# Kernel optimization log

Measured on AMD Instinct MI355X. Metric: run time of the kernel, lower is better.

Reference implementation:

```python
import jax, jax.numpy as jnp
import numpy as np

N = 50000      # nodes
E = 400000     # edges
NODE_IN = 16
EDGE_IN = 8
H = 4          # heads (layer 1)
C = 64         # hidden_dim
HC = H * C     # 256


def setup_inputs() -> dict:
    key = jax.random.key(0)
    ks = iter(jax.random.split(key, 48))
    def rn(shape, s=0.05):
        return jax.random.normal(next(ks), shape, jnp.float32) * s
    x = jax.random.normal(next(ks), (N, NODE_IN), jnp.float32)
    edge_index = jax.random.randint(next(ks), (2, E), 0, N)
    edge_attr = jax.random.normal(next(ks), (E, EDGE_IN), jnp.float32)
    params = dict(
        # conv1: GATv2Conv(node_in -> hidden, heads=4, concat=True, edge_dim=edge_in)
        Wl1=rn((NODE_IN, HC)), bl1=jnp.zeros((HC,), jnp.float32),
        Wr1=rn((NODE_IN, HC)), br1=jnp.zeros((HC,), jnp.float32),
        We1=rn((EDGE_IN, HC)), att1=rn((H, C)), bias1=jnp.zeros((HC,), jnp.float32),
        # conv2: GATv2Conv(hidden*heads -> hidden, heads=1, concat=False)
        Wl2=rn((HC, C)), bl2=jnp.zeros((C,), jnp.float32),
        Wr2=rn((HC, C)), br2=jnp.zeros((C,), jnp.float32),
        We2=rn((EDGE_IN, C)), att2=rn((1, C)), bias2=jnp.zeros((C,), jnp.float32),
        # batchnorms (eval mode: running stats)
        bn1_g=jnp.ones((HC,), jnp.float32), bn1_b=jnp.zeros((HC,), jnp.float32),
        bn1_m=rn((HC,), 0.01), bn1_v=jnp.ones((HC,), jnp.float32),
        bn2_g=jnp.ones((C,), jnp.float32), bn2_b=jnp.zeros((C,), jnp.float32),
        bn2_m=rn((C,), 0.01), bn2_v=jnp.ones((C,), jnp.float32),
        # residual projection
        Wres=rn((NODE_IN, HC)),
        Wm1=rn((2 * C + EDGE_IN, C)), bm1=jnp.zeros((C,), jnp.float32),
        Wm2=rn((C, C // 2)), bm2=jnp.zeros((C // 2,), jnp.float32),
        Wm3=rn((C // 2, 1)), bm3=jnp.zeros((1,), jnp.float32),
    )
    return dict(x=x, edge_index=edge_index, edge_attr=edge_attr, **params)


def _gatv2(x, src, dst, e_attr, Wl, bl, Wr, br, We, att, bias, heads, out_ch, concat):
    """GATv2Conv message passing (PyG semantics, self-loops already in src/dst)."""
    n = x.shape[0]
    xl = (x @ Wl + bl).reshape(n, heads, out_ch)   # source transform
    xr = (x @ Wr + br).reshape(n, heads, out_ch)   # target transform
    ee = (e_attr @ We).reshape(-1, heads, out_ch)  # edge transform
    # per-edge attention logits: leaky_relu(x_i + x_j + e) . att
    m = jax.nn.leaky_relu(xl[src] + xr[dst] + ee, 0.2)        # [Etot, H, C]
    alpha = jnp.einsum('ehc,hc->eh', m, att)                  # [Etot, H]
    # segment softmax over destination nodes (every node has a self-loop)
    amax = jax.ops.segment_max(alpha, dst, num_segments=n)    # [N, H]
    expa = jnp.exp(alpha - amax[dst])
    denom = jax.ops.segment_sum(expa, dst, num_segments=n)    # [N, H]
    a = expa / (denom[dst] + 1e-16)
    out = jax.ops.segment_sum(xl[src] * a[:, :, None], dst, num_segments=n)  # [N, H, C]
    out = out.reshape(n, heads * out_ch) if concat else out.mean(axis=1)
    return out + bias


def _bn(h, g, b, m, v):
    return (h - m) * jax.lax.rsqrt(v + 1e-5) * g + b


def _forward(x, edge_attr, Wl1, bl1, Wr1, br1, We1, att1, bias1,
             Wl2, bl2, Wr2, br2, We2, att2, bias2,
             bn1_g, bn1_b, bn1_m, bn1_v, bn2_g, bn2_b, bn2_m, bn2_v,
             Wres, Wm1, bm1, Wm2, bm2, Wm3, bm3, edge_index):
    row, col = edge_index[0], edge_index[1]
    # add self-loops with fill_value='mean' for edge_attr (GATv2Conv default)
    loop = jnp.arange(N)
    src = jnp.concatenate([row, loop])
    dst = jnp.concatenate([col, loop])
    ea_mean = edge_attr.mean(axis=0, keepdims=True)
    ea_full = jnp.concatenate([edge_attr, jnp.broadcast_to(ea_mean, (N, EDGE_IN))], axis=0)
    h = _gatv2(x, src, dst, ea_full, Wl1, bl1, Wr1, br1, We1, att1, bias1, H, C, True)
    h = _bn(h, bn1_g, bn1_b, bn1_m, bn1_v)
    h = jax.nn.elu(h + x @ Wres)                 # residual; dropout is a no-op in eval
    h = _gatv2(h, src, dst, ea_full, Wl2, bl2, Wr2, br2, We2, att2, bias2, 1, C, False)
    h = _bn(h, bn2_g, bn2_b, bn2_m, bn2_v)
    h = jax.nn.elu(h)
    # edge head: gather endpoint embeddings + edge_attr -> MLP -> sigmoid
    er = jnp.concatenate([h[row], h[col], edge_attr], axis=-1)   # [E, 2C+edge_in]
    z = jax.nn.gelu(er @ Wm1 + bm1, approximate=False)
    z = jax.nn.gelu(z @ Wm2 + bm2, approximate=False)
    return jax.nn.sigmoid(z @ Wm3 + bm3)[:, 0]                    # [E]


def reference(x, edge_index, edge_attr, Wl1, bl1, Wr1, br1, We1, att1, bias1,
              Wl2, bl2, Wr2, br2, We2, att2, bias2,
              bn1_g, bn1_b, bn1_m, bn1_v, bn2_g, bn2_b, bn2_m, bn2_v,
              Wres, Wm1, bm1, Wm2, bm2, Wm3, bm3):
    return _forward(x, edge_attr, Wl1, bl1, Wr1, br1, We1, att1, bias1,
                    Wl2, bl2, Wr2, br2, We2, att2, bias2,
                    bn1_g, bn1_b, bn1_m, bn1_v, bn2_g, bn2_b, bn2_m, bn2_v,
                    Wres, Wm1, bm1, Wm2, bm2, Wm3, bm3, edge_index)
```

## Files before the change

### kernel.cpp

```cpp
#include <hip/hip_runtime.h>
#include <hip/hip_bf16.h>
#include <hip/hip_fp16.h>
#include <math.h>

#define NN 50000
#define EE 400000
#define ETOT (NN + EE)

__device__ __forceinline__ float gelu_f(float x) {
    return 0.5f * x * (1.f + erff(x * 0.7071067811865476f));
}
__device__ __forceinline__ float elu_f(float x) {
    return x > 0.f ? x : expm1f(x);
}
__device__ __forceinline__ float4 half8_lo_hi(uint4 raw, float4* hi) {
    __half2 h0 = *(__half2*)&raw.x, h1 = *(__half2*)&raw.y;
    __half2 h2 = *(__half2*)&raw.z, h3 = *(__half2*)&raw.w;
    float2 f0 = __half22float2(h0), f1 = __half22float2(h1);
    float2 f2 = __half22float2(h2), f3 = __half22float2(h3);
    *hi = make_float4(f2.x, f2.y, f3.x, f3.y);
    return make_float4(f0.x, f0.y, f1.x, f1.y);
}

__global__ __launch_bounds__(256) void k_init(const float* __restrict__ ea, float* __restrict__ ea_sum,
                                              const int* __restrict__ ei, int* __restrict__ counts,
                                              int E, int N) {
    int t = threadIdx.x;
    if (blockIdx.x < 256) {
        float s[8];
#pragma unroll
        for (int i = 0; i < 8; i++) s[i] = 0.f;
        for (int e = blockIdx.x * 256 + t; e < E; e += 256 * 256) {
            const float4* p = (const float4*)(ea + (size_t)e * 8);
            float4 a = p[0], b = p[1];
            s[0] += a.x; s[1] += a.y; s[2] += a.z; s[3] += a.w;
            s[4] += b.x; s[5] += b.y; s[6] += b.z; s[7] += b.w;
        }
#pragma unroll
        for (int o = 32; o; o >>= 1)
#pragma unroll
            for (int i = 0; i < 8; i++) s[i] += __shfl_xor(s[i], o, 64);
        __shared__ float sh[4][8];
        int lane = t & 63, w = t >> 6;
        if (lane == 0)
#pragma unroll
            for (int i = 0; i < 8; i++) sh[w][i] = s[i];
        __syncthreads();
        if (t < 8) {
            float v = sh[0][t] + sh[1][t] + sh[2][t] + sh[3][t];
            atomicAdd(ea_sum + t, v);
        }
    } else {
        int e = (blockIdx.x - 256) * 256 + t;
        if (e >= E + N) return;
        int d = (e < E) ? ei[E + e] : (e - E);
        atomicAdd(counts + d, 1);
    }
}

__global__ __launch_bounds__(1024) void k_scan(const int* __restrict__ counts, int* __restrict__ off,
                                               int* __restrict__ cursor, int N) {
    __shared__ int buf[1024];
    int t = threadIdx.x;
    int carry = 0;
    if (t == 0) off[0] = 0;
    for (int base = 0; base < N; base += 4096) {
        int i0 = base + t * 4;
        int v0 = 0, v1 = 0, v2 = 0, v3 = 0;
        if (i0 + 3 < N) {
            int4 vv = *(const int4*)(counts + i0);
            v0 = vv.x; v1 = vv.y; v2 = vv.z; v3 = vv.w;
        } else {
            if (i0 < N)     v0 = counts[i0];
            if (i0 + 1 < N) v1 = counts[i0 + 1];
            if (i0 + 2 < N) v2 = counts[i0 + 2];
            if (i0 + 3 < N) v3 = counts[i0 + 3];
        }
        int s01 = v0 + v1, s012 = s01 + v2, tot4 = s012 + v3;
        buf[t] = tot4;
        __syncthreads();
        for (int o = 1; o < 1024; o <<= 1) {
            int add = (t >= o) ? buf[t - o] : 0;
            __syncthreads();
            buf[t] += add;
            __syncthreads();
        }
        int incl4 = buf[t] + carry;
        int excl = incl4 - tot4;
        if (i0 < N)     { off[i0 + 1] = excl + v0;   cursor[i0]     = excl; }
        if (i0 + 1 < N) { off[i0 + 2] = excl + s01;  cursor[i0 + 1] = excl + v0; }
        if (i0 + 2 < N) { off[i0 + 3] = excl + s012; cursor[i0 + 2] = excl + s01; }
        if (i0 + 3 < N) { off[i0 + 4] = excl + tot4; cursor[i0 + 3] = excl + s012; }
        int tot = buf[1023];
        __syncthreads();
        carry += tot;
    }
}

__global__ __launch_bounds__(256) void k_scat_nt1(const int* __restrict__ ei, int* __restrict__ cursor,
                                                  int* __restrict__ csr_src, int* __restrict__ csr_eid,
                                                  const float* __restrict__ x,
                                                  const float* __restrict__ Wl, const float* __restrict__ bl,
                                                  const float* __restrict__ Wr, const float* __restrict__ br,
                                                  __half* __restrict__ xl1h, float* __restrict__ xr1,
                                                  int E, int N) {
    __shared__ float swl[16 * 256];
    __shared__ float swr[16 * 256];
    __shared__ float sx[32 * 16];
    int t = threadIdx.x;
    int S = (E + N + 255) >> 8;
    if ((int)blockIdx.x < S) {
        int e = blockIdx.x * 256 + t;
        if (e >= E + N) return;
        int s, d;
        if (e < E) { s = ei[e]; d = ei[E + e]; }
        else { s = d = e - E; }
        int pos = atomicAdd(cursor + d, 1);
        csr_src[pos] = s;
        csr_eid[pos] = e;
        return;
    }
    int bid = blockIdx.x - S;
#pragma unroll
    for (int k = 0; k < 16; k++) { swl[k * 256 + t] = Wl[k * 256 + t]; swr[k * 256 + t] = Wr[k * 256 + t]; }
    int n0 = bid * 32;
    for (int i = t; i < 32 * 16; i += 256) {
        int n = n0 + (i >> 4);
        sx[i] = (n < N) ? x[(size_t)n * 16 + (i & 15)] : 0.f;
    }
    __syncthreads();
    float bL = bl[t], bR = br[t];
    for (int ni = 0; ni < 32; ni++) {
        int n = n0 + ni;
        if (n >= N) break;
        float al = bL, ar = bR;
#pragma unroll
        for (int k = 0; k < 16; k++) {
            float xv = sx[ni * 16 + k];
            al += xv * swl[k * 256 + t];
            ar += xv * swr[k * 256 + t];
        }
        xl1h[(size_t)n * 256 + t] = __float2half(al);
        xr1[(size_t)n * 256 + t] = ar;
    }
}

__global__ __launch_bounds__(256) void k_fagg1(const __half* __restrict__ xl1h, const float* __restrict__ xr1,
                                               const int* __restrict__ off, const int* __restrict__ csr_src,
                                               const int* __restrict__ csr_eid,
                                               const float* __restrict__ ea, const float* __restrict__ ea_sum,
                                               const float* __restrict__ We1, const float* __restrict__ att1,
                                               const float* __restrict__ bias1,
                                               const float* __restrict__ x, const float* __restrict__ Wres,
                                               const float* __restrict__ g, const float* __restrict__ bb_,
                                               const float* __restrict__ mm_, const float* __restrict__ vv_,
                                               float* __restrict__ h1,
                                               int E, int N) {
    int t = threadIdx.x;
    int lane = t & 63, w = t >> 6;
    int node = blockIdx.x * 4 + w;
    if (node >= N) return;
    int c4 = lane * 4;
    float4 we[8];
#pragma unroll
    for (int k = 0; k < 8; k++) we[k] = *(const float4*)(We1 + k * 256 + c4);
    float4 xr4 = *(const float4*)(xr1 + (size_t)node * 256 + c4);
    float4 at4 = *(const float4*)(att1 + c4);
    float invE = 1.f / (float)E;
    float4 eam0, eam1;
    eam0.x = ea_sum[0] * invE; eam0.y = ea_sum[1] * invE;
    eam0.z = ea_sum[2] * invE; eam0.w = ea_sum[3] * invE;
    eam1.x = ea_sum[4] * invE; eam1.y = ea_sum[5] * invE;
    eam1.z = ea_sum[6] * invE; eam1.w = ea_sum[7] * invE;

    int beg = off[node], end = off[node + 1];
    float m = -1e30f, sumw = 0.f;
    float4 acc = make_float4(0.f, 0.f, 0.f, 0.f);

    int cb = beg;
    while (cb < end) {
        int cnt = end - cb; if (cnt > 64) cnt = 64;
        int sl = 0;
        float4 ba = eam0, bb4 = eam1;
        if (lane < cnt) {
            sl = csr_src[cb + lane];
            int el = csr_eid[cb + lane];
            if (el < E) {
                ba  = *(const float4*)(ea + (size_t)el * 8);
                bb4 = *(const float4*)(ea + (size_t)el * 8 + 4);
            }
        }
        float2 r0 = make_float2(0.f, 0.f), r1 = r0, r2 = r0;
        {
            int s0 = __shfl(sl, 0, 64);
            r0 = *(const float2*)(xl1h + (size_t)s0 * 256 + c4);
            if (cnt > 1) { int s1 = __shfl(sl, 1, 64); r1 = *(const float2*)(xl1h + (size_t)s1 * 256 + c4); }
            if (cnt > 2) { int s2 = __shfl(sl, 2, 64); r2 = *(const float2*)(xl1h + (size_t)s2 * 256 + c4); }
        }
        for (int j = 0; j < cnt; j++) {
            float2 cur = r0;
            r0 = r1; r1 = r2;
            if (j + 3 < cnt) {
                int s3 = __shfl(sl, j + 3, 64);
                r2 = *(const float2*)(xl1h + (size_t)s3 * 256 + c4);
            }
            float eav[8];
            eav[0] = __shfl(ba.x, j, 64);  eav[1] = __shfl(ba.y, j, 64);
            eav[2] = __shfl(ba.z, j, 64);  eav[3] = __shfl(ba.w, j, 64);
            eav[4] = __shfl(bb4.x, j, 64); eav[5] = __shfl(bb4.y, j, 64);
            eav[6] = __shfl(bb4.z, j, 64); eav[7] = __shfl(bb4.w, j, 64);
            const __half2* hp = (const __half2*)&cur;
            float2 lo = __half22float2(hp[0]);
            float2 hi = __half22float2(hp[1]);
            float4 xs = make_float4(lo.x, lo.y, hi.x, hi.y);
            float4 ee = make_float4(0.f, 0.f, 0.f, 0.f);
#pragma unroll
            for (int k = 0; k < 8; k++) {
                ee.x += eav[k] * we[k].x; ee.y += eav[k] * we[k].y;
                ee.z += eav[k] * we[k].z; ee.w += eav[k] * we[k].w;
            }
            float4 v;
            v.x = xs.x + xr4.x + ee.x; v.y = xs.y + xr4.y + ee.y;
            v.z = xs.z + xr4.z + ee.z; v.w = xs.w + xr4.w + ee.w;
            v.x = v.x > 0.f ? v.x : 0.2f * v.x;
            v.y = v.y > 0.f ? v.y : 0.2f * v.y;
            v.z = v.z > 0.f ? v.z : 0.2f * v.z;
            v.w = v.w > 0.f ? v.w : 0.2f * v.w;
            float p = v.x * at4.x + v.y * at4.y + v.z * at4.z + v.w * at4.w;
            p += __shfl_xor(p, 1, 64);
            p += __shfl_xor(p, 2, 64);
            p += __shfl_xor(p, 4, 64);
            p += __shfl_xor(p, 8, 64);
            float mn = fmaxf(m, p);
            float sc = expf(m - mn);
            float wgt = expf(p - mn);
            acc.x = acc.x * sc + wgt * xs.x;
            acc.y = acc.y * sc + wgt * xs.y;
            acc.z = acc.z * sc + wgt * xs.z;
            acc.w = acc.w * sc + wgt * xs.w;
            sumw = sumw * sc + wgt;
            m = mn;
        }
        cb += cnt;
    }
    float inv = 1.f / (sumw + 1e-16f);
    float4 r = make_float4(0.f, 0.f, 0.f, 0.f);
#pragma unroll
    for (int q = 0; q < 4; q++) {
        float4 xq = *(const float4*)(x + (size_t)node * 16 + q * 4);
        float xa[4] = { xq.x, xq.y, xq.z, xq.w };
#pragma unroll
        for (int kk = 0; kk < 4; kk++) {
            float4 wv = *(const float4*)(Wres + (size_t)(q * 4 + kk) * 256 + c4);
            r.x += xa[kk] * wv.x; r.y += xa[kk] * wv.y;
            r.z += xa[kk] * wv.z; r.w += xa[kk] * wv.w;
        }
    }
    float4 bi = *(const float4*)(bias1 + c4);
    float4 g4 = *(const float4*)(g + c4);
    float4 b4 = *(const float4*)(bb_ + c4);
    float4 m4 = *(const float4*)(mm_ + c4);
    float4 v4 = *(const float4*)(vv_ + c4);
    float4 o;
    o.x = acc.x * inv + bi.x; o.y = acc.y * inv + bi.y;
    o.z = acc.z * inv + bi.z; o.w = acc.w * inv + bi.w;
    o.x = (o.x - m4.x) * rsqrtf(v4.x + 1e-5f) * g4.x + b4.x + r.x;
    o.y = (o.y - m4.y) * rsqrtf(v4.y + 1e-5f) * g4.y + b4.y + r.y;
    o.z = (o.z - m4.z) * rsqrtf(v4.z + 1e-5f) * g4.z + b4.z + r.z;
    o.w = (o.w - m4.w) * rsqrtf(v4.w + 1e-5f) * g4.w + b4.w + r.w;
    o.x = elu_f(o.x); o.y = elu_f(o.y); o.z = elu_f(o.z); o.w = elu_f(o.w);
    *(float4*)(h1 + (size_t)node * 256 + c4) = o;
}

__global__ __launch_bounds__(256) void k_xlr2(const float* __restrict__ h1,
                                              const float* __restrict__ Wl2, const float* __restrict__ bl2,
                                              const float* __restrict__ Wr2, const float* __restrict__ br2,
                                              __half* __restrict__ xl2h, float* __restrict__ xr2, int N) {
    __shared__ float sh[32][32];
    __shared__ float sw[32][128];
    int t = threadIdx.x;
    int tr = t >> 5, tc = t & 31;
    int n0 = blockIdx.x * 32;
    float acc[4][4];
#pragma unroll
    for (int i = 0; i < 4; i++)
#pragma unroll
        for (int j = 0; j < 4; j++) acc[i][j] = 0.f;
    for (int k0 = 0; k0 < 256; k0 += 32) {
        {
            int n = t >> 3, kk0 = (t & 7) * 4;
            int gn = n0 + n;
            float4 hv = make_float4(0.f, 0.f, 0.f, 0.f);
            if (gn < N) hv = *(const float4*)(h1 + (size_t)gn * 256 + k0 + kk0);
            sh[kk0 + 0][n] = hv.x; sh[kk0 + 1][n] = hv.y; sh[kk0 + 2][n] = hv.z; sh[kk0 + 3][n] = hv.w;
        }
        for (int i = t; i < 32 * 128; i += 256) {
            int kk = i >> 7, c = i & 127;
            sw[kk][c] = (c < 64) ? Wl2[(size_t)(k0 + kk) * 64 + c] : Wr2[(size_t)(k0 + kk) * 64 + (c - 64)];
        }
        __syncthreads();
#pragma unroll
        for (int kk = 0; kk < 32; kk++) {
            float4 hv = *(const float4*)&sh[kk][tr * 4];
            float4 wv = *(const float4*)&sw[kk][tc * 4];
            float hh[4] = { hv.x, hv.y, hv.z, hv.w };
            float wwv[4] = { wv.x, wv.y, wv.z, wv.w };
#pragma unroll
            for (int i = 0; i < 4; i++)
#pragma unroll
                for (int j = 0; j < 4; j++) acc[i][j] += hh[i] * wwv[j];
        }
        __syncthreads();
    }
#pragma unroll
    for (int i = 0; i < 4; i++) {
        int gn = n0 + tr * 4 + i;
        if (gn >= N) continue;
#pragma unroll
        for (int j = 0; j < 4; j++) {
            int c = tc * 4 + j;
            float vv = acc[i][j];
            if (c < 64) xl2h[(size_t)gn * 64 + c] = __float2half(vv + bl2[c]);
            else        xr2[(size_t)gn * 64 + (c - 64)] = vv + br2[c - 64];
        }
    }
}

__global__ __launch_bounds__(256) void k_fagg2(const __half* __restrict__ xl2h, const float* __restrict__ xr2,
                                               const int* __restrict__ off, const int* __restrict__ csr_src,
                                               const int* __restrict__ csr_eid,
                                               const float* __restrict__ ea, const float* __restrict__ ea_sum,
                                               const float* __restrict__ We2, const float* __restrict__ att2,
                                               const float* __restrict__ bias2,
                                               const float* __restrict__ g, const float* __restrict__ bb_,
                                               const float* __restrict__ mm_, const float* __restrict__ vv_,
                                               __half* __restrict__ h2h,
                                               int E, int N) {
    int t = threadIdx.x;
    int lane = t & 63, w = t >> 6;
    int node = blockIdx.x * 4 + w;
    if (node >= N) return;
    float we[8];
#pragma unroll
    for (int k = 0; k < 8; k++) we[k] = We2[k * 64 + lane];
    float xr = xr2[(size_t)node * 64 + lane];
    float at = att2[lane];
    float invE = 1.f / (float)E;
    float4 eam0, eam1;
    eam0.x = ea_sum[0] * invE; eam0.y = ea_sum[1] * invE;
    eam0.z = ea_sum[2] * invE; eam0.w = ea_sum[3] * invE;
    eam1.x = ea_sum[4] * invE; eam1.y = ea_sum[5] * invE;
    eam1.z = ea_sum[6] * invE; eam1.w = ea_sum[7] * invE;

    int beg = off[node], end = off[node + 1];
    float m = -1e30f, sumw = 0.f, acc = 0.f;

    int cb = beg;
    while (cb < end) {
        int cnt = end - cb; if (cnt > 64) cnt = 64;
        int sl = 0;
        float4 ba = eam0, bb4 = eam1;
        if (lane < cnt) {
            sl = csr_src[cb + lane];
            int el = csr_eid[cb + lane];
            if (el < E) {
                ba  = *(const float4*)(ea + (size_t)el * 8);
                bb4 = *(const float4*)(ea + (size_t)el * 8 + 4);
            }
        }
        float r0 = 0.f, r1 = 0.f, r2 = 0.f;
        {
            int s0 = __shfl(sl, 0, 64);
            r0 = __half2float(xl2h[(size_t)s0 * 64 + lane]);
            if (cnt > 1) { int s1 = __shfl(sl, 1, 64); r1 = __half2float(xl2h[(size_t)s1 * 64 + lane]); }
            if (cnt > 2) { int s2 = __shfl(sl, 2, 64); r2 = __half2float(xl2h[(size_t)s2 * 64 + lane]); }
        }
        for (int j = 0; j < cnt; j++) {
            float xs = r0;
            r0 = r1; r1 = r2;
            if (j + 3 < cnt) {
                int s3 = __shfl(sl, j + 3, 64);
                r2 = __half2float(xl2h[(size_t)s3 * 64 + lane]);
            }
            float eav[8];
            eav[0] = __shfl(ba.x, j, 64);  eav[1] = __shfl(ba.y, j, 64);
            eav[2] = __shfl(ba.z, j, 64);  eav[3] = __shfl(ba.w, j, 64);
            eav[4] = __shfl(bb4.x, j, 64); eav[5] = __shfl(bb4.y, j, 64);
            eav[6] = __shfl(bb4.z, j, 64); eav[7] = __shfl(bb4.w, j, 64);
            float v = xs + xr;
#pragma unroll
            for (int k = 0; k < 8; k++) v += eav[k] * we[k];
            v = v > 0.f ? v : 0.2f * v;
            float p = v * at;
#pragma unroll
            for (int o = 32; o; o >>= 1) p += __shfl_xor(p, o, 64);
            float mn = fmaxf(m, p);
            float sc = expf(m - mn);
            float wgt = expf(p - mn);
            acc = acc * sc + wgt * xs;
            sumw = sumw * sc + wgt;
            m = mn;
        }
        cb += cnt;
    }
    float val = acc / (sumw + 1e-16f) + bias2[lane];
    val = (val - mm_[lane]) * rsqrtf(vv_[lane] + 1e-5f) * g[lane] + bb_[lane];
    h2h[(size_t)node * 64 + lane] = __float2half(elu_f(val));
}

__global__ __launch_bounds__(256) void k_uv(const __half* __restrict__ h2h, const float* __restrict__ Wm1,
                                            __half* __restrict__ uh, __half* __restrict__ vh, int N) {
    __shared__ float sh[32][32];
    __shared__ float sw[32][128];
    int t = threadIdx.x;
    int tr = t >> 5, tc = t & 31;
    int n0 = blockIdx.x * 32;
    float acc[4][4];
#pragma unroll
    for (int i = 0; i < 4; i++)
#pragma unroll
        for (int j = 0; j < 4; j++) acc[i][j] = 0.f;
    for (int k0 = 0; k0 < 64; k0 += 32) {
        {
            int n = t >> 3, kk0 = (t & 7) * 4;
            int gn = n0 + n;
            float4 hv = make_float4(0.f, 0.f, 0.f, 0.f);
            if (gn < N) {
                uint2 raw = *(const uint2*)(h2h + (size_t)gn * 64 + k0 + kk0);
                __half2 a = *(__half2*)&raw.x, b = *(__half2*)&raw.y;
                float2 fa = __half22float2(a), fb = __half22float2(b);
                hv = make_float4(fa.x, fa.y, fb.x, fb.y);
            }
            sh[kk0 + 0][n] = hv.x; sh[kk0 + 1][n] = hv.y; sh[kk0 + 2][n] = hv.z; sh[kk0 + 3][n] = hv.w;
        }
        for (int i = t; i < 32 * 128; i += 256) {
            int kk = i >> 7, c = i & 127;
            sw[kk][c] = (c < 64) ? Wm1[(size_t)(k0 + kk) * 64 + c]
                                 : Wm1[(size_t)(64 + k0 + kk) * 64 + (c - 64)];
        }
        __syncthreads();
#pragma unroll
        for (int kk = 0; kk < 32; kk++) {
            float4 hv = *(const float4*)&sh[kk][tr * 4];
            float4 wv = *(const float4*)&sw[kk][tc * 4];
            float hh[4] = { hv.x, hv.y, hv.z, hv.w };
            float wwv[4] = { wv.x, wv.y, wv.z, wv.w };
#pragma unroll
            for (int i = 0; i < 4; i++)
#pragma unroll
                for (int j = 0; j < 4; j++) acc[i][j] += hh[i] * wwv[j];
        }
        __syncthreads();
    }
#pragma unroll
    for (int i = 0; i < 4; i++) {
        int gn = n0 + tr * 4 + i;
        if (gn >= N) continue;
#pragma unroll
        for (int j = 0; j < 4; j++) {
            int c = tc * 4 + j;
            if (c < 64) uh[(size_t)gn * 64 + c] = __float2half(acc[i][j]);
            else        vh[(size_t)gn * 64 + (c - 64)] = __float2half(acc[i][j]);
        }
    }
}

__global__ __launch_bounds__(256) void k_mlp2(const __half* __restrict__ uh, const __half* __restrict__ vh,
                                              const float* __restrict__ ea, const int* __restrict__ ei,
                                              const float* __restrict__ Wm1, const float* __restrict__ bm1,
                                              const float* __restrict__ Wm2, const float* __restrict__ bm2,
                                              const float* __restrict__ Wm3, const float* __restrict__ bm3,
                                              float* __restrict__ out, int E) {
    __shared__ float sw2[64 * 32];
    __shared__ float sW1e[8 * 64];
    __shared__ float sb1[64];
    __shared__ int sre[64], sce[64];
    __shared__ float z1[64 * 68];
    int t = threadIdx.x;
    for (int i = t; i < 64 * 32; i += 256) sw2[i] = Wm2[i];
    for (int i = t; i < 512; i += 256) sW1e[i] = Wm1[128 * 64 + i];
    if (t < 64) sb1[t] = bm1[t];
    int e0 = blockIdx.x * 64;
    if (t < 64) {
        int e = e0 + t;
        if (e < E) { sre[t] = ei[e]; sce[t] = ei[E + e]; }
        else { sre[t] = 0; sce[t] = 0; }
    }
    __syncthreads();
    for (int i = t; i < 512; i += 256) {
        int el = i >> 3, q = i & 7;
        int r = sre[el], c = sce[el];
        uint4 ru = *(const uint4*)(uh + (size_t)r * 64 + q * 8);
        uint4 rv = *(const uint4*)(vh + (size_t)c * 64 + q * 8);
        float4 a0 = *(const float4*)(ea + (size_t)(e0 + el) * 8);
        float4 a1 = *(const float4*)(ea + (size_t)(e0 + el) * 8 + 4);
        float av[8] = { a0.x, a0.y, a0.z, a0.w, a1.x, a1.y, a1.z, a1.w };
        float wv[8];
#pragma unroll
        for (int j = 0; j < 8; j++) wv[j] = sb1[q * 8 + j];
#pragma unroll
        for (int k = 0; k < 8; k++) {
            float a = av[k];
#pragma unroll
            for (int j = 0; j < 8; j++) wv[j] += a * sW1e[k * 64 + q * 8 + j];
        }
        float4 uhi, vhi;
        float4 ulo = half8_lo_hi(ru, &uhi);
        float4 vlo = half8_lo_hi(rv, &vhi);
        float4 zlo, zhi;
        zlo.x = gelu_f(ulo.x + vlo.x + wv[0]);
        zlo.y = gelu_f(ulo.y + vlo.y + wv[1]);
        zlo.z = gelu_f(ulo.z + vlo.z + wv[2]);
        zlo.w = gelu_f(ulo.w + vlo.w + wv[3]);
        zhi.x = gelu_f(uhi.x + vhi.x + wv[4]);
        zhi.y = gelu_f(uhi.y + vhi.y + wv[5]);
        zhi.z = gelu_f(uhi.z + vhi.z + wv[6]);
        zhi.w = gelu_f(uhi.w + vhi.w + wv[7]);
        *(float4*)(z1 + el * 68 + q * 8)     = zlo;
        *(float4*)(z1 + el * 68 + q * 8 + 4) = zhi;
    }
    __syncthreads();
    int tr = t >> 3;
    int tc = t & 7;
    float b2[4], w3[4];
#pragma unroll
    for (int j = 0; j < 4; j++) { b2[j] = bm2[tc * 4 + j]; w3[j] = Wm3[tc * 4 + j]; }
    float b3 = bm3[0];
    float acc0[4], acc1[4];
#pragma unroll
    for (int j = 0; j < 4; j++) { acc0[j] = 0.f; acc1[j] = 0.f; }
    const float* z0p = z1 + (tr * 2 + 0) * 68;
    const float* z1p = z1 + (tr * 2 + 1) * 68;
#pragma unroll 8
    for (int k = 0; k < 64; k++) {
        float4 wv = *(const float4*)(sw2 + k * 32 + tc * 4);
        float a0 = z0p[k];
        float a1 = z1p[k];
        acc0[0] += a0 * wv.x; acc0[1] += a0 * wv.y; acc0[2] += a0 * wv.z; acc0[3] += a0 * wv.w;
        acc1[0] += a1 * wv.x; acc1[1] += a1 * wv.y; acc1[2] += a1 * wv.z; acc1[3] += a1 * wv.w;
    }
    float p0 = 0.f, p1 = 0.f;
#pragma unroll
    for (int j = 0; j < 4; j++) {
        p0 += gelu_f(acc0[j] + b2[j]) * w3[j];
        p1 += gelu_f(acc1[j] + b2[j]) * w3[j];
    }
    p0 += __shfl_xor(p0, 1, 64); p0 += __shfl_xor(p0, 2, 64); p0 += __shfl_xor(p0, 4, 64);
    p1 += __shfl_xor(p1, 1, 64); p1 += __shfl_xor(p1, 2, 64); p1 += __shfl_xor(p1, 4, 64);
    if (tc == 0) {
        int e = e0 + tr * 2;
        if (e < E)     out[e]     = 1.f / (1.f + expf(-(p0 + b3)));
        if (e + 1 < E) out[e + 1] = 1.f / (1.f + expf(-(p1 + b3)));
    }
}

extern "C" void kernel_launch(void* const* d_in, const int* in_sizes, int n_in,
                              void* d_out, int out_size, void* d_ws, size_t ws_size,
                              hipStream_t stream) {
    const float* x    = (const float*)d_in[0];
    const int*   ei   = (const int*)d_in[1];
    const float* ea   = (const float*)d_in[2];
    const float* Wl1  = (const float*)d_in[3];
    const float* bl1  = (const float*)d_in[4];
    const float* Wr1  = (const float*)d_in[5];
    const float* br1  = (const float*)d_in[6];
    const float* We1  = (const float*)d_in[7];
    const float* att1 = (const float*)d_in[8];
    const float* bias1= (const float*)d_in[9];
    const float* Wl2  = (const float*)d_in[10];
    const float* bl2  = (const float*)d_in[11];
    const float* Wr2  = (const float*)d_in[12];
    const float* br2  = (const float*)d_in[13];
    const float* We2  = (const float*)d_in[14];
    const float* att2 = (const float*)d_in[15];
    const float* bias2= (const float*)d_in[16];
    const float* bn1g = (const float*)d_in[17];
    const float* bn1b = (const float*)d_in[18];
    const float* bn1m = (const float*)d_in[19];
    const float* bn1v = (const float*)d_in[20];
    const float* bn2g = (const float*)d_in[21];
    const float* bn2b = (const float*)d_in[22];
    const float* bn2m = (const float*)d_in[23];
    const float* bn2v = (const float*)d_in[24];
    const float* Wres = (const float*)d_in[25];
    const float* Wm1  = (const float*)d_in[26];
    const float* bm1  = (const float*)d_in[27];
    const float* Wm2  = (const float*)d_in[28];
    const float* bm2  = (const float*)d_in[29];
    const float* Wm3  = (const float*)d_in[30];
    const float* bm3  = (const float*)d_in[31];
    float* out = (float*)d_out;
    float* ws = (float*)d_ws;

    const int N = NN, E = EE, Etot = ETOT;

    float* ea_sum   = ws;
    int*   counts   = (int*)(ws + 16);
    int*   off      = (int*)(ws + 16 + (size_t)N);
    int*   cursor   = (int*)(ws + 32 + (size_t)2 * N);
    int*   csr_src  = (int*)(ws + 32 + (size_t)3 * N);
    int*   csr_eid  = (int*)(ws + 32 + (size_t)3 * N + Etot);
    size_t base     = 32 + (size_t)3 * N + (size_t)2 * Etot;
    __half* xl1h    = (__half*)(ws + base);
    __half* xl2h    = xl1h;
    __half* h2h     = (__half*)(ws + base + (size_t)128 * N);
    float* xr1      = ws + base + (size_t)160 * N;
    float* h1       = xr1;
    float* xr2      = xr1 + (size_t)256 * N;
    __half* uh      = (__half*)xr2;
    __half* vh      = uh + (size_t)64 * N;

    hipMemsetAsync(ea_sum, 0, 16 * sizeof(float), stream);
    hipMemsetAsync(counts, 0, (size_t)N * sizeof(int), stream);

    int S = (Etot + 255) / 256;
    k_init<<<256 + S, 256, 0, stream>>>(ea, ea_sum, ei, counts, E, N);
    k_scan<<<1, 1024, 0, stream>>>(counts, off, cursor, N);
    k_scat_nt1<<<S + (N + 31) / 32, 256, 0, stream>>>(ei, cursor, csr_src, csr_eid,
                                                      x, Wl1, bl1, Wr1, br1, xl1h, xr1, E, N);
    k_fagg1<<<(N + 3) / 4, 256, 0, stream>>>(xl1h, xr1, off, csr_src, csr_eid, ea, ea_sum,
                                             We1, att1, bias1, x, Wres,
                                             bn1g, bn1b, bn1m, bn1v, h1, E, N);
    k_xlr2<<<(N + 31) / 32, 256, 0, stream>>>(h1, Wl2, bl2, Wr2, br2, xl2h, xr2, N);
    k_fagg2<<<(N + 3) / 4, 256, 0, stream>>>(xl2h, xr2, off, csr_src, csr_eid, ea, ea_sum,
                                             We2, att2, bias2,
                                             bn2g, bn2b, bn2m, bn2v, h2h, E, N);
    k_uv<<<(N + 31) / 32, 256, 0, stream>>>(h2h, Wm1, uh, vh, N);
    k_mlp2<<<(E + 63) / 64, 256, 0, stream>>>(uh, vh, ea, ei, Wm1, bm1, Wm2, bm2, Wm3, bm3, out, E);
}
```

Baseline: 506.1 us.

## Process four edges per wavefront iteration in layer-2 aggregation with online-softmax merge

The layer-2 GATv2 aggregation kernel now splits each 64-lane wavefront into four 16-lane segments. Each segment handles a different incoming edge and each lane covers four channels. Per-segment online-softmax states are then merged across segments with xor shuffles before the final bias, batchnorm and ELU. This cuts the sequential edge loop length and the full-wave reduction depth by about four times, and vectorises the feature gathers. The cost is extra exp work in the merge and idle segments on the tail of each chunk.

```diff
diff --git a/kernel.cpp b/kernel.cpp
--- a/kernel.cpp
+++ b/kernel.cpp
@@ -340,11 +340,13 @@
     int lane = t & 63, w = t >> 6;
     int node = blockIdx.x * 4 + w;
     if (node >= N) return;
-    float we[8];
-#pragma unroll
-    for (int k = 0; k < 8; k++) we[k] = We2[k * 64 + lane];
-    float xr = xr2[(size_t)node * 64 + lane];
-    float at = att2[lane];
+    int seg = lane >> 4;
+    int c4 = (lane & 15) * 4;
+    float4 we[8];
+#pragma unroll
+    for (int k = 0; k < 8; k++) we[k] = *(const float4*)(We2 + k * 64 + c4);
+    float4 xr4 = *(const float4*)(xr2 + (size_t)node * 64 + c4);
+    float4 at4 = *(const float4*)(att2 + c4);
     float invE = 1.f / (float)E;
     float4 eam0, eam1;
     eam0.x = ea_sum[0] * invE; eam0.y = ea_sum[1] * invE;
@@ -353,7 +355,8 @@
     eam1.z = ea_sum[6] * invE; eam1.w = ea_sum[7] * invE;
 
     int beg = off[node], end = off[node + 1];
-    float m = -1e30f, sumw = 0.f, acc = 0.f;
+    float m = -1e30f, sumw = 0.f;
+    float4 acc = make_float4(0.f, 0.f, 0.f, 0.f);
 
     int cb = beg;
     while (cb < end) {
@@ -368,44 +371,101 @@
                 bb4 = *(const float4*)(ea + (size_t)el * 8 + 4);
             }
         }
-        float r0 = 0.f, r1 = 0.f, r2 = 0.f;
+        int nit = (cnt + 3) >> 2;
+        float2 r0, r1;
         {
-            int s0 = __shfl(sl, 0, 64);
-            r0 = __half2float(xl2h[(size_t)s0 * 64 + lane]);
-            if (cnt > 1) { int s1 = __shfl(sl, 1, 64); r1 = __half2float(xl2h[(size_t)s1 * 64 + lane]); }
-            if (cnt > 2) { int s2 = __shfl(sl, 2, 64); r2 = __half2float(xl2h[(size_t)s2 * 64 + lane]); }
-        }
-        for (int j = 0; j < cnt; j++) {
-            float xs = r0;
-            r0 = r1; r1 = r2;
-            if (j + 3 < cnt) {
-                int s3 = __shfl(sl, j + 3, 64);
-                r2 = __half2float(xl2h[(size_t)s3 * 64 + lane]);
+            int s0 = __shfl(sl, seg, 64);
+            r0 = *(const float2*)(xl2h + (size_t)s0 * 64 + c4);
+            int s1 = __shfl(sl, (seg + 4) & 63, 64);
+            r1 = *(const float2*)(xl2h + (size_t)s1 * 64 + c4);
+        }
+        for (int it = 0; it < nit; ++it) {
+            int jj = it * 4 + seg;
+            float2 cur = r0;
+            r0 = r1;
+            {
+                int sn = __shfl(sl, (jj + 8) & 63, 64);
+                r1 = *(const float2*)(xl2h + (size_t)sn * 64 + c4);
             }
             float eav[8];
-            eav[0] = __shfl(ba.x, j, 64);  eav[1] = __shfl(ba.y, j, 64);
-            eav[2] = __shfl(ba.z, j, 64);  eav[3] = __shfl(ba.w, j, 64);
-            eav[4] = __shfl(bb4.x, j, 64); eav[5] = __shfl(bb4.y, j, 64);
-            eav[6] = __shfl(bb4.z, j, 64); eav[7] = __shfl(bb4.w, j, 64);
-            float v = xs + xr;
-#pragma unroll
-            for (int k = 0; k < 8; k++) v += eav[k] * we[k];
-            v = v > 0.f ? v : 0.2f * v;
-            float p = v * at;
-#pragma unroll
-            for (int o = 32; o; o >>= 1) p += __shfl_xor(p, o, 64);
-            float mn = fmaxf(m, p);
+            eav[0] = __shfl(ba.x, jj, 64);  eav[1] = __shfl(ba.y, jj, 64);
+            eav[2] = __shfl(ba.z, jj, 64);  eav[3] = __shfl(ba.w, jj, 64);
+            eav[4] = __shfl(bb4.x, jj, 64); eav[5] = __shfl(bb4.y, jj, 64);
+            eav[6] = __shfl(bb4.z, jj, 64); eav[7] = __shfl(bb4.w, jj, 64);
+            const __half2* hp = (const __half2*)&cur;
+            float2 lo = __half22float2(hp[0]);
+            float2 hi = __half22float2(hp[1]);
+            float4 xs = make_float4(lo.x, lo.y, hi.x, hi.y);
+            float4 ee = make_float4(0.f, 0.f, 0.f, 0.f);
+#pragma unroll
+            for (int k = 0; k < 8; k++) {
+                ee.x += eav[k] * we[k].x; ee.y += eav[k] * we[k].y;
+                ee.z += eav[k] * we[k].z; ee.w += eav[k] * we[k].w;
+            }
+            float4 v;
+            v.x = xs.x + xr4.x + ee.x; v.y = xs.y + xr4.y + ee.y;
+            v.z = xs.z + xr4.z + ee.z; v.w = xs.w + xr4.w + ee.w;
+            v.x = v.x > 0.f ? v.x : 0.2f * v.x;
+            v.y = v.y > 0.f ? v.y : 0.2f * v.y;
+            v.z = v.z > 0.f ? v.z : 0.2f * v.z;
+            v.w = v.w > 0.f ? v.w : 0.2f * v.w;
+            float p = v.x * at4.x + v.y * at4.y + v.z * at4.z + v.w * at4.w;
+            p += __shfl_xor(p, 1, 64);
+            p += __shfl_xor(p, 2, 64);
+            p += __shfl_xor(p, 4, 64);
+            p += __shfl_xor(p, 8, 64);
+            bool valid = jj < cnt;
+            float pe = valid ? p : -1e30f;
+            float mn = fmaxf(m, pe);
             float sc = expf(m - mn);
-            float wgt = expf(p - mn);
-            acc = acc * sc + wgt * xs;
+            float wgt = valid ? expf(pe - mn) : 0.f;
+            acc.x = acc.x * sc + wgt * xs.x;
+            acc.y = acc.y * sc + wgt * xs.y;
+            acc.z = acc.z * sc + wgt * xs.z;
+            acc.w = acc.w * sc + wgt * xs.w;
             sumw = sumw * sc + wgt;
             m = mn;
         }
         cb += cnt;
     }
-    float val = acc / (sumw + 1e-16f) + bias2[lane];
-    val = (val - mm_[lane]) * rsqrtf(vv_[lane] + 1e-5f) * g[lane] + bb_[lane];
-    h2h[(size_t)node * 64 + lane] = __float2half(elu_f(val));
+#pragma unroll
+    for (int d = 16; d <= 32; d <<= 1) {
+        float m2 = __shfl_xor(m, d, 64);
+        float s2 = __shfl_xor(sumw, d, 64);
+        float ax = __shfl_xor(acc.x, d, 64);
+        float ay = __shfl_xor(acc.y, d, 64);
+        float az = __shfl_xor(acc.z, d, 64);
+        float aw = __shfl_xor(acc.w, d, 64);
+        float mn = fmaxf(m, m2);
+        float e1 = expf(m - mn), e2 = expf(m2 - mn);
+        acc.x = acc.x * e1 + ax * e2;
+        acc.y = acc.y * e1 + ay * e2;
+        acc.z = acc.z * e1 + az * e2;
+        acc.w = acc.w * e1 + aw * e2;
+        sumw = sumw * e1 + s2 * e2;
+        m = mn;
+    }
+    float inv = 1.f / (sumw + 1e-16f);
+    float4 bi = *(const float4*)(bias2 + c4);
+    float4 g4 = *(const float4*)(g + c4);
+    float4 b4 = *(const float4*)(bb_ + c4);
+    float4 m4 = *(const float4*)(mm_ + c4);
+    float4 v4 = *(const float4*)(vv_ + c4);
+    float4 o;
+    o.x = acc.x * inv + bi.x; o.y = acc.y * inv + bi.y;
+    o.z = acc.z * inv + bi.z; o.w = acc.w * inv + bi.w;
+    o.x = (o.x - m4.x) * rsqrtf(v4.x + 1e-5f) * g4.x + b4.x;
+    o.y = (o.y - m4.y) * rsqrtf(v4.y + 1e-5f) * g4.y + b4.y;
+    o.z = (o.z - m4.z) * rsqrtf(v4.z + 1e-5f) * g4.z + b4.z;
+    o.w = (o.w - m4.w) * rsqrtf(v4.w + 1e-5f) * g4.w + b4.w;
+    if (seg == 0) {
+        __half2 h0 = __floats2half2_rn(elu_f(o.x), elu_f(o.y));
+        __half2 h1 = __floats2half2_rn(elu_f(o.z), elu_f(o.w));
+        uint2 pk;
+        pk.x = *(unsigned*)&h0;
+        pk.y = *(unsigned*)&h1;
+        *(uint2*)(h2h + (size_t)node * 64 + c4) = pk;
+    }
 }
 
 __global__ __launch_bounds__(256) void k_uv(const __half* __restrict__ h2h, const float* __restrict__ Wm1,
```

Result: faster. 482.2 us (-4.7%).
